# Kernel tuning notes

Hardware: AMD Instinct MI355X
Metric: run time of the kernel (lower is better)

Reference implementation:

```python
import jax, jax.numpy as jnp
import numpy as np


def setup_inputs() -> dict:
    B, S, D = 4, 4096, 256
    key = jax.random.key(0)
    ks = jax.random.split(key, 7)
    s = 1.0 / np.sqrt(D)
    return {
        "x": jax.random.normal(ks[0], (B, S, D), dtype=jnp.float32),
        "Wq": jax.random.normal(ks[1], (D, D), dtype=jnp.float32) * s,
        "bq": jnp.zeros((D,), dtype=jnp.float32),
        "Wk": jax.random.normal(ks[2], (D, D), dtype=jnp.float32) * s,
        "bk": jnp.zeros((D,), dtype=jnp.float32),
        "Wv": jax.random.normal(ks[3], (D, D), dtype=jnp.float32) * s,
        "bv": jnp.zeros((D,), dtype=jnp.float32),
    }


def reference(x, Wq, bq, Wk, bk, Wv, bv):
    # Dense projections (single head, no scaling in original)
    Q = x @ Wq + bq  # [B,S,D]
    K = x @ Wk + bk
    V = x @ Wv + bv
    scores = jnp.einsum("bsd,btd->bst", Q, K)  # [B,S,S]
    # Original takes top_k with k = seq_len, so threshold == row minimum;
    # mask 'scores >= threshold' keeps everything (no-op), kept for fidelity.
    threshold = jnp.min(scores, axis=-1, keepdims=True)
    NEG = jnp.float32(-1e9)
    sparse_scores = jnp.where(scores >= threshold, scores, NEG)
    weights = jax.nn.softmax(sparse_scores, axis=-1)
    return jnp.einsum("bst,btd->bsd", weights, V)  # [B,S,D]
```

## Files before the change

### kernel.cpp

```cpp
#include <hip/hip_runtime.h>
#include <hip/hip_fp16.h>


typedef _Float16 f16x8 __attribute__((ext_vector_type(8)));
typedef _Float16 f16x4 __attribute__((ext_vector_type(4)));
typedef __fp16   fp16x2 __attribute__((ext_vector_type(2)));
typedef float    f32x4 __attribute__((ext_vector_type(4)));
typedef float    f32x16 __attribute__((ext_vector_type(16)));

#define MFMA16(A, B, C) __builtin_amdgcn_mfma_f32_16x16x32_f16((A), (B), (C), 0, 0, 0)
#define MFMA32(A, B, C) __builtin_amdgcn_mfma_f32_32x32x16_f16((A), (B), (C), 0, 0, 0)

static __device__ __forceinline__ void gload16(const _Float16* g, _Float16* l) {
    __builtin_amdgcn_global_load_lds(
        (unsigned int __attribute__((address_space(1)))*)g,
        (unsigned int __attribute__((address_space(3)))*)l, 16, 0, 0);
}

static __device__ __forceinline__ unsigned packh(float a, float b) {
    union { fp16x2 h; unsigned u; } x;
    x.h = __builtin_amdgcn_cvt_pkrtz(a, b);
    return x.u;
}

static __device__ __forceinline__ float fexp2(float x) {
    float r;
    asm("v_exp_f32 %0, %1" : "=v"(r) : "v"(x));
    return r;
}

static __device__ __forceinline__ void load_xfrag(const float* xp, f16x8& Ah, f16x8& Al) {
    float4 a0 = *(const float4*)xp;
    float4 a1 = *(const float4*)(xp + 4);
    float v[8] = {a0.x, a0.y, a0.z, a0.w, a1.x, a1.y, a1.z, a1.w};
#pragma unroll
    for (int j = 0; j < 8; ++j) {
        _Float16 h = (_Float16)v[j];
        Ah[j] = h;
        Al[j] = (_Float16)(v[j] - (float)h);
    }
}

static __device__ __forceinline__ void load_xfrag_hi(const float* xp, f16x8& Ah) {
    float4 a0 = *(const float4*)xp;
    float4 a1 = *(const float4*)(xp + 4);
    float v[8] = {a0.x, a0.y, a0.z, a0.w, a1.x, a1.y, a1.z, a1.w};
#pragma unroll
    for (int j = 0; j < 8; ++j) Ah[j] = (_Float16)v[j];
}

__global__ __launch_bounds__(256) void convert_w_kernel(
    const float* __restrict__ Wq, const float* __restrict__ Wk, const float* __restrict__ Wv,
    _Float16* __restrict__ Wth, _Float16* __restrict__ Wtl, int* __restrict__ cnt)
{
    if (blockIdx.x == 0 && threadIdx.x < 8) cnt[threadIdx.x * 64] = 0;
    int idx = blockIdx.x * 256 + threadIdx.x;
    int mat = idx >> 16, e = idx & 65535;
    int k = e >> 8, n = e & 255;
    const float* W = (mat == 0) ? Wq : (mat == 1) ? Wk : Wv;
    float v = W[e];
    _Float16 h = (_Float16)v;
    _Float16 lo = (_Float16)(v - (float)h);
    const int lane = (n & 15) + 16 * ((k >> 3) & 3);
    const int dst = mat * 65536 + (((k >> 5) * 16 + (n >> 4)) * 64 + lane) * 8 + (k & 7);
    Wth[dst] = h;
    Wtl[dst] = lo;
}

template <int MODE>
static __device__ __forceinline__ void proj_body(
    const float* __restrict__ x, const _Float16* __restrict__ Wh,
    const _Float16* __restrict__ Wl, const float* __restrict__ bias,
    _Float16* __restrict__ dst)
{
    const int tid = threadIdx.x, wid = tid >> 6, lane = tid & 63;
    const int lrow = lane & 15, lgrp = lane >> 4;
    const int rb = blockIdx.x * 4 + wid;
    const int row0 = rb * 16;

    f32x4 acc[16];
#pragma unroll
    for (int i = 0; i < 16; ++i) acc[i] = f32x4{0.f, 0.f, 0.f, 0.f};

#pragma unroll
    for (int ks = 0; ks < 8; ++ks) {
        f16x8 Ah, Al;
        if constexpr (MODE == 2) {
            load_xfrag_hi(x + (size_t)(row0 + lrow) * 256 + ks * 32 + lgrp * 8, Ah);
        } else {
            load_xfrag(x + (size_t)(row0 + lrow) * 256 + ks * 32 + lgrp * 8, Ah, Al);
        }
#pragma unroll
        for (int nt = 0; nt < 16; ++nt) {
            const size_t bbase = ((ks * 16 + nt) * 64 + lane) * 8;
            f16x8 Bh = *(const f16x8*)(Wh + bbase);
            acc[nt] = MFMA16(Ah, Bh, acc[nt]);
            if constexpr (MODE != 2) {
                f16x8 Bl = *(const f16x8*)(Wl + bbase);
                acc[nt] = MFMA16(Al, Bh, acc[nt]);
                acc[nt] = MFMA16(Ah, Bl, acc[nt]);
            }
        }
    }

    const float LOG2E = 1.4426950408889634f;
#pragma unroll
    for (int nt = 0; nt < 16; ++nt) {
        const int n = nt * 16 + lrow;
        const float bb = bias[n];
        if constexpr (MODE == 2) {
            const int m0 = row0 + lgrp * 4;
            f16x4 vv;
#pragma unroll
            for (int r = 0; r < 4; ++r) vv[r] = (_Float16)(acc[nt][r] + bb);
            *(f16x4*)(dst + (size_t)n * 16384 + m0) = vv;
        } else {
            const float s = (MODE == 0) ? LOG2E : 1.0f;
#pragma unroll
            for (int r = 0; r < 4; ++r) {
                const int grow = row0 + lgrp * 4 + r;
                dst[(size_t)grow * 256 + n] = (_Float16)((acc[nt][r] + bb) * s);
            }
        }
    }
}

__global__ __launch_bounds__(256) void proj_all_kernel(
    const float* __restrict__ x,
    const _Float16* __restrict__ Wth, const _Float16* __restrict__ Wtl,
    const float* __restrict__ bq, const float* __restrict__ bk,
    const float* __restrict__ bv,
    _Float16* __restrict__ Qf, _Float16* __restrict__ Kf, _Float16* __restrict__ Vt)
{
    const int m = blockIdx.y;
    if (m == 0)      proj_body<0>(x, Wth,          Wtl,          bq, Qf);
    else if (m == 1) proj_body<1>(x, Wth + 65536,  Wtl + 65536,  bk, Kf);
    else             proj_body<2>(x, Wth + 131072, nullptr,      bv, Vt);
}

__global__ __launch_bounds__(256, 2) void attn8_kernel(
    const _Float16* __restrict__ Qf, const _Float16* __restrict__ Kf,
    const _Float16* __restrict__ Vt, _Float16* __restrict__ Op01,
    _Float16* __restrict__ Op23, float* __restrict__ ml, int* __restrict__ cnt)
{
    __shared__ _Float16 Kb[2][32 * 256];
    __shared__ _Float16 Vb[2][256 * 32];
    __shared__ int s_item;

    const int tid = threadIdx.x, wid = tid >> 6, lane = tid & 63;
    const int lq = lane & 31, hi = lane >> 5;

    if (tid == 0) {
        int xcd;
        asm volatile("s_getreg_b32 %0, hwreg(HW_REG_XCC_ID)" : "=s"(xcd));
        xcd &= 7;
        int item = -1;
#pragma unroll 1
        for (int k = 0; k < 8; ++k) {
            const int qidx = (xcd + k) & 7;
            int v = atomicAdd(cnt + qidx * 64, 1);
            if (v < 64) { item = qidx * 64 + v; break; }
        }
        s_item = item;
    }
    __syncthreads();
    const int item = s_item;
    const int group = (item >> 6) * 2 + ((item & 63) >> 5);
    const int qi = item & 31;
    const int b = group >> 2, split = group & 3;
    const size_t bS = (size_t)b * 4096;
    const size_t qrow = bS + qi * 128 + wid * 32;
    const size_t k0g = bS + (size_t)split * 1024;
    const int NT = 32;

    f16x8 QB[16];
#pragma unroll
    for (int ks = 0; ks < 16; ++ks)
        QB[ks] = *(const f16x8*)(Qf + (qrow + lq) * 256 + ks * 16 + hi * 8);

    f32x16 Oacc[8];
#pragma unroll
    for (int i = 0; i < 8; ++i)
#pragma unroll
        for (int r = 0; r < 16; ++r) Oacc[i][r] = 0.f;
    float m_r = -1e30f, l_r = 0.f;

    auto stage = [&](int buf, int t) {
        const size_t krow = k0g + (size_t)t * 32;
#pragma unroll
        for (int it = 0; it < 4; ++it) {
            const int s = it * 256 + tid;
            const int row = s >> 5, c = s & 31;
            const int src = c ^ (row & 7) ^ (((row >> 3) & 3) << 3);
            gload16(Kf + (krow + row) * 256 + src * 8, &Kb[buf][s * 8]);
        }
#pragma unroll
        for (int it = 0; it < 4; ++it) {
            const int s = it * 256 + tid;
            const int d = s >> 2, c = s & 3;
            gload16(Vt + (size_t)d * 16384 + krow + ((c ^ ((d >> 1) & 3)) * 8), &Vb[buf][s * 8]);
        }
    };

    stage(0, 0);
    asm volatile("s_waitcnt vmcnt(0)" ::: "memory");
    __builtin_amdgcn_s_barrier();

    const float THR = 10.0f;
    const int kx = (lq & 7) ^ (((lq >> 3) & 3) << 3);
    const int vx = (lq >> 1) & 3;
    int buf = 0;
    for (int t = 0; t < NT; ++t) {
        if (t + 1 < NT) stage(buf ^ 1, t + 1);
        const _Float16* K_ = Kb[buf];
        const _Float16* V_ = Vb[buf];

        f32x16 sc;
#pragma unroll
        for (int r = 0; r < 16; ++r) sc[r] = 0.f;
#pragma unroll
        for (int ks = 0; ks < 16; ++ks) {
            const int slot = (2 * ks + hi) ^ kx;
            f16x8 Ak = *(const f16x8*)((const char*)K_ + lq * 512 + slot * 16);
            sc = MFMA32(Ak, QB[ks], sc);
        }

        float tm[8];
#pragma unroll
        for (int j = 0; j < 8; ++j) tm[j] = fmaxf(sc[j], sc[j + 8]);
#pragma unroll
        for (int s = 4; s > 0; s >>= 1)
#pragma unroll
            for (int j = 0; j < s; ++j) tm[j] = fmaxf(tm[j], tm[j + s]);
        float mx = fmaxf(tm[0], __shfl_xor(tm[0], 32));
        if (__any(mx > m_r + THR)) {
            const float mn = fmaxf(m_r, mx);
            const float scl = fexp2(m_r - mn);
            m_r = mn; l_r *= scl;
#pragma unroll
            for (int i = 0; i < 8; ++i)
#pragma unroll
                for (int r = 0; r < 16; ++r) Oacc[i][r] *= scl;
        }

        float p[16];
#pragma unroll
        for (int r = 0; r < 16; ++r) p[r] = fexp2(sc[r] - m_r);
        float ts[8];
#pragma unroll
        for (int j = 0; j < 8; ++j) ts[j] = p[j] + p[j + 8];
#pragma unroll
        for (int s = 4; s > 0; s >>= 1)
#pragma unroll
            for (int j = 0; j < s; ++j) ts[j] += ts[j + s];
        l_r += ts[0] + __shfl_xor(ts[0], 32);

        unsigned w[8], pw[8];
#pragma unroll
        for (int j = 0; j < 8; ++j) {
            w[j] = packh(p[2 * j], p[2 * j + 1]);
            pw[j] = __shfl_xor(w[j], 32);
        }
        f16x8 Pfrag[2];
#pragma unroll
        for (int s = 0; s < 2; ++s) {
            unsigned f0 = hi ? pw[4 * s + 2] : w[4 * s + 0];
            unsigned f1 = hi ? pw[4 * s + 3] : w[4 * s + 1];
            unsigned f2 = hi ? w[4 * s + 2] : pw[4 * s + 0];
            unsigned f3 = hi ? w[4 * s + 3] : pw[4 * s + 1];
            union { unsigned u[4]; f16x8 f; } cvt;
            cvt.u[0] = f0; cvt.u[1] = f1; cvt.u[2] = f2; cvt.u[3] = f3;
            Pfrag[s] = cvt.f;
        }

#pragma unroll
        for (int dblk = 0; dblk < 8; ++dblk) {
#pragma unroll
            for (int kstep = 0; kstep < 2; ++kstep) {
                const int slot = (kstep * 2 + hi) ^ vx;
                f16x8 Av = *(const f16x8*)((const char*)V_ + (dblk * 32 + lq) * 64 + slot * 16);
                Oacc[dblk] = MFMA32(Av, Pfrag[kstep], Oacc[dblk]);
            }
        }

        asm volatile("s_waitcnt vmcnt(0)" ::: "memory");
        __builtin_amdgcn_s_barrier();
        buf ^= 1;
    }

    _Float16* Ops = (split < 2) ? (Op01 + (size_t)split * 4194304)
                                : (Op23 + (size_t)(split - 2) * 4194304);
    const float inv = 1.0f / l_r;
    const size_t grow = qrow + lq;
#pragma unroll
    for (int dblk = 0; dblk < 8; ++dblk)
#pragma unroll
        for (int quad = 0; quad < 4; ++quad) {
            f16x4 o;
#pragma unroll
            for (int j = 0; j < 4; ++j) o[j] = (_Float16)(Oacc[dblk][quad * 4 + j] * inv);
            *(f16x4*)(Ops + grow * 256 + dblk * 32 + 8 * quad + 4 * hi) = o;
        }
    if (hi == 0) {
        ml[((size_t)split * 16384 + grow) * 2]     = m_r;
        ml[((size_t)split * 16384 + grow) * 2 + 1] = l_r;
    }
}

__global__ __launch_bounds__(256) void combine_kernel(
    const _Float16* __restrict__ Op01, const _Float16* __restrict__ Op23,
    const float* __restrict__ ml, float* __restrict__ out)
{
    const int idx = blockIdx.x * 256 + threadIdx.x;
    const int row = idx >> 3, d8 = (idx & 7) * 32;
    float m_s[4], l_s[4], w[4];
    float M = -1e30f;
#pragma unroll
    for (int s = 0; s < 4; ++s) {
        m_s[s] = ml[((size_t)s * 16384 + row) * 2];
        l_s[s] = ml[((size_t)s * 16384 + row) * 2 + 1];
        M = fmaxf(M, m_s[s]);
    }
    float Wsum = 0.f;
#pragma unroll
    for (int s = 0; s < 4; ++s) { w[s] = l_s[s] * fexp2(m_s[s] - M); Wsum += w[s]; }
    const float inv = 1.0f / Wsum;
#pragma unroll
    for (int s = 0; s < 4; ++s) w[s] *= inv;

#pragma unroll
    for (int ch = 0; ch < 4; ++ch) {
        const int d0 = d8 + ch * 8;
        float acc[8] = {0.f, 0.f, 0.f, 0.f, 0.f, 0.f, 0.f, 0.f};
#pragma unroll
        for (int s = 0; s < 4; ++s) {
            const _Float16* Op = (s < 2) ? (Op01 + (size_t)s * 4194304)
                                         : (Op23 + (size_t)(s - 2) * 4194304);
            f16x8 v = *(const f16x8*)(Op + (size_t)row * 256 + d0);
#pragma unroll
            for (int j = 0; j < 8; ++j) acc[j] += w[s] * (float)v[j];
        }
        float4 o0 = {acc[0], acc[1], acc[2], acc[3]};
        float4 o1 = {acc[4], acc[5], acc[6], acc[7]};
        *(float4*)(out + (size_t)row * 256 + d0) = o0;
        *(float4*)(out + (size_t)row * 256 + d0 + 4) = o1;
    }
}

extern "C" void kernel_launch(void* const* d_in, const int* in_sizes, int n_in,
                              void* d_out, int out_size, void* d_ws, size_t ws_size,
                              hipStream_t stream) {
    const float* x  = (const float*)d_in[0];
    const float* Wq = (const float*)d_in[1];
    const float* bq = (const float*)d_in[2];
    const float* Wk = (const float*)d_in[3];
    const float* bk = (const float*)d_in[4];
    const float* Wv = (const float*)d_in[5];
    const float* bv = (const float*)d_in[6];
    float* out = (float*)d_out;

    _Float16* Op01 = (_Float16*)d_ws;
    _Float16* Qf  = Op01 + 2 * 4194304;
    _Float16* Kf  = Qf  + 4194304;
    _Float16* Vt  = Kf  + 4194304;
    _Float16* Wth = Vt  + 4194304;
    _Float16* Wtl = Wth + 196608;
    float*    ml  = (float*)(Wtl + 196608);
    _Float16* Op23 = (_Float16*)((char*)ml + 524288);
    int*      cnt = (int*)(Op23 + 2 * 4194304);

    convert_w_kernel<<<768, 256, 0, stream>>>(Wq, Wk, Wv, Wth, Wtl, cnt);
    proj_all_kernel<<<dim3(256, 3), 256, 0, stream>>>(x, Wth, Wtl, bq, bk, bv, Qf, Kf, Vt);
    attn8_kernel<<<512, 256, 0, stream>>>(Qf, Kf, Vt, Op01, Op23, ml, cnt);
    combine_kernel<<<512, 256, 0, stream>>>(Op01, Op23, ml, out);
}
```

Measured before the change: 166.9 us.

## Fuse combine into attention, drop split-fp16 projections, stage projection stores via LDS

Removes the fp16 hi/lo error-compensation terms for the Q and K projections, cutting projection MFMAs threefold and dropping the low-part weight buffer. The weight conversion kernel now writes whole 8-element fragments per thread. Projection outputs are staged through LDS so global stores are coalesced 16-byte writes. The separate combine kernel is replaced by a last-block-done pattern inside the attention kernel using a done counter and threadfence. This saves a launch but loses some precision on Q and K.

New measurement: 242.6 us. +45.3%, slower.

```diff
diff --git a/kernel.cpp b/kernel.cpp
--- a/kernel.cpp
+++ b/kernel.cpp
@@ -29,18 +29,6 @@
     return r;
 }
 
-static __device__ __forceinline__ void load_xfrag(const float* xp, f16x8& Ah, f16x8& Al) {
-    float4 a0 = *(const float4*)xp;
-    float4 a1 = *(const float4*)(xp + 4);
-    float v[8] = {a0.x, a0.y, a0.z, a0.w, a1.x, a1.y, a1.z, a1.w};
-#pragma unroll
-    for (int j = 0; j < 8; ++j) {
-        _Float16 h = (_Float16)v[j];
-        Ah[j] = h;
-        Al[j] = (_Float16)(v[j] - (float)h);
-    }
-}
-
 static __device__ __forceinline__ void load_xfrag_hi(const float* xp, f16x8& Ah) {
     float4 a0 = *(const float4*)xp;
     float4 a1 = *(const float4*)(xp + 4);
@@ -51,27 +39,30 @@
 
 __global__ __launch_bounds__(256) void convert_w_kernel(
     const float* __restrict__ Wq, const float* __restrict__ Wk, const float* __restrict__ Wv,
-    _Float16* __restrict__ Wth, _Float16* __restrict__ Wtl, int* __restrict__ cnt)
+    _Float16* __restrict__ Wth, int* __restrict__ cnt, int* __restrict__ done)
 {
-    if (blockIdx.x == 0 && threadIdx.x < 8) cnt[threadIdx.x * 64] = 0;
+    if (blockIdx.x == 0) {
+        if (threadIdx.x < 8)   cnt[threadIdx.x * 64] = 0;
+        if (threadIdx.x < 128) done[threadIdx.x * 16] = 0;
+    }
     int idx = blockIdx.x * 256 + threadIdx.x;
-    int mat = idx >> 16, e = idx & 65535;
-    int k = e >> 8, n = e & 255;
+    int mat = idx >> 13, f_l = idx & 8191;
+    int frag = f_l >> 6, lane = f_l & 63;
+    int ks = frag >> 4, nt = frag & 15;
+    int n = nt * 16 + (lane & 15);
+    int k0 = ks * 32 + ((lane >> 4) & 3) * 8;
     const float* W = (mat == 0) ? Wq : (mat == 1) ? Wk : Wv;
-    float v = W[e];
-    _Float16 h = (_Float16)v;
-    _Float16 lo = (_Float16)(v - (float)h);
-    const int lane = (n & 15) + 16 * ((k >> 3) & 3);
-    const int dst = mat * 65536 + (((k >> 5) * 16 + (n >> 4)) * 64 + lane) * 8 + (k & 7);
-    Wth[dst] = h;
-    Wtl[dst] = lo;
+    f16x8 h;
+#pragma unroll
+    for (int j = 0; j < 8; ++j) h[j] = (_Float16)W[(k0 + j) * 256 + n];
+    *(f16x8*)(Wth + mat * 65536 + (size_t)f_l * 8) = h;
 }
 
 template <int MODE>
 static __device__ __forceinline__ void proj_body(
     const float* __restrict__ x, const _Float16* __restrict__ Wh,
-    const _Float16* __restrict__ Wl, const float* __restrict__ bias,
-    _Float16* __restrict__ dst)
+    const float* __restrict__ bias, _Float16* __restrict__ dst,
+    _Float16* __restrict__ lds)
 {
     const int tid = threadIdx.x, wid = tid >> 6, lane = tid & 63;
     const int lrow = lane & 15, lgrp = lane >> 4;
@@ -84,64 +75,77 @@
 
 #pragma unroll
     for (int ks = 0; ks < 8; ++ks) {
-        f16x8 Ah, Al;
-        if constexpr (MODE == 2) {
-            load_xfrag_hi(x + (size_t)(row0 + lrow) * 256 + ks * 32 + lgrp * 8, Ah);
-        } else {
-            load_xfrag(x + (size_t)(row0 + lrow) * 256 + ks * 32 + lgrp * 8, Ah, Al);
-        }
+        f16x8 Ah;
+        load_xfrag_hi(x + (size_t)(row0 + lrow) * 256 + ks * 32 + lgrp * 8, Ah);
 #pragma unroll
         for (int nt = 0; nt < 16; ++nt) {
-            const size_t bbase = ((ks * 16 + nt) * 64 + lane) * 8;
-            f16x8 Bh = *(const f16x8*)(Wh + bbase);
+            f16x8 Bh = *(const f16x8*)(Wh + ((ks * 16 + nt) * 64 + lane) * 8);
             acc[nt] = MFMA16(Ah, Bh, acc[nt]);
-            if constexpr (MODE != 2) {
-                f16x8 Bl = *(const f16x8*)(Wl + bbase);
-                acc[nt] = MFMA16(Al, Bh, acc[nt]);
-                acc[nt] = MFMA16(Ah, Bl, acc[nt]);
+        }
+    }
+
+    const float LOG2E = 1.4426950408889634f;
+    if constexpr (MODE == 2) {
+        const int m_l = wid * 16 + lgrp * 4;
+        const int cm = m_l >> 3, oic = (lgrp & 1) * 4;
+#pragma unroll
+        for (int nt = 0; nt < 16; ++nt) {
+            const int n = nt * 16 + lrow;
+            const float bb = bias[n];
+            f16x4 v;
+#pragma unroll
+            for (int r = 0; r < 4; ++r) v[r] = (_Float16)(acc[nt][r] + bb);
+            *(f16x4*)(lds + n * 72 + (cm ^ (n & 7)) * 8 + oic) = v;
+        }
+        __syncthreads();
+#pragma unroll
+        for (int it = 0; it < 8; ++it) {
+            const int u = it * 256 + tid;
+            const int n = u >> 3, c = u & 7;
+            f16x8 v = *(const f16x8*)(lds + n * 72 + ((c ^ (n & 7))) * 8);
+            *(f16x8*)(dst + (size_t)n * 16384 + blockIdx.x * 64 + c * 8) = v;
+        }
+    } else {
+        const float s = (MODE == 0) ? LOG2E : 1.0f;
+#pragma unroll
+        for (int nt = 0; nt < 16; ++nt) {
+            const int n = nt * 16 + lrow;
+            const float bb = bias[n];
+#pragma unroll
+            for (int r = 0; r < 4; ++r) {
+                const int row_l = wid * 16 + lgrp * 4 + r;
+                lds[row_l * 264 + n] = (_Float16)((acc[nt][r] + bb) * s);
             }
         }
-    }
-
-    const float LOG2E = 1.4426950408889634f;
-#pragma unroll
-    for (int nt = 0; nt < 16; ++nt) {
-        const int n = nt * 16 + lrow;
-        const float bb = bias[n];
-        if constexpr (MODE == 2) {
-            const int m0 = row0 + lgrp * 4;
-            f16x4 vv;
-#pragma unroll
-            for (int r = 0; r < 4; ++r) vv[r] = (_Float16)(acc[nt][r] + bb);
-            *(f16x4*)(dst + (size_t)n * 16384 + m0) = vv;
-        } else {
-            const float s = (MODE == 0) ? LOG2E : 1.0f;
-#pragma unroll
-            for (int r = 0; r < 4; ++r) {
-                const int grow = row0 + lgrp * 4 + r;
-                dst[(size_t)grow * 256 + n] = (_Float16)((acc[nt][r] + bb) * s);
-            }
+        __syncthreads();
+#pragma unroll
+        for (int it = 0; it < 8; ++it) {
+            const int u = it * 256 + tid;
+            const int row_l = u >> 5, c = u & 31;
+            f16x8 v = *(const f16x8*)(lds + row_l * 264 + c * 8);
+            *(f16x8*)(dst + ((size_t)blockIdx.x * 64 + row_l) * 256 + c * 8) = v;
         }
     }
 }
 
 __global__ __launch_bounds__(256) void proj_all_kernel(
-    const float* __restrict__ x,
-    const _Float16* __restrict__ Wth, const _Float16* __restrict__ Wtl,
+    const float* __restrict__ x, const _Float16* __restrict__ Wth,
     const float* __restrict__ bq, const float* __restrict__ bk,
     const float* __restrict__ bv,
     _Float16* __restrict__ Qf, _Float16* __restrict__ Kf, _Float16* __restrict__ Vt)
 {
+    __shared__ _Float16 lds[18432];
     const int m = blockIdx.y;
-    if (m == 0)      proj_body<0>(x, Wth,          Wtl,          bq, Qf);
-    else if (m == 1) proj_body<1>(x, Wth + 65536,  Wtl + 65536,  bk, Kf);
-    else             proj_body<2>(x, Wth + 131072, nullptr,      bv, Vt);
+    if (m == 0)      proj_body<0>(x, Wth,          bq, Qf, lds);
+    else if (m == 1) proj_body<1>(x, Wth + 65536,  bk, Kf, lds);
+    else             proj_body<2>(x, Wth + 131072, bv, Vt, lds);
 }
 
 __global__ __launch_bounds__(256, 2) void attn8_kernel(
     const _Float16* __restrict__ Qf, const _Float16* __restrict__ Kf,
     const _Float16* __restrict__ Vt, _Float16* __restrict__ Op01,
-    _Float16* __restrict__ Op23, float* __restrict__ ml, int* __restrict__ cnt)
+    _Float16* __restrict__ Op23, float* __restrict__ ml, int* __restrict__ cnt,
+    int* __restrict__ done, float* __restrict__ out)
 {
     __shared__ _Float16 Kb[2][32 * 256];
     __shared__ _Float16 Vb[2][256 * 32];
@@ -305,45 +309,48 @@
         ml[((size_t)split * 16384 + grow) * 2]     = m_r;
         ml[((size_t)split * 16384 + grow) * 2 + 1] = l_r;
     }
-}
-
-__global__ __launch_bounds__(256) void combine_kernel(
-    const _Float16* __restrict__ Op01, const _Float16* __restrict__ Op23,
-    const float* __restrict__ ml, float* __restrict__ out)
-{
-    const int idx = blockIdx.x * 256 + threadIdx.x;
-    const int row = idx >> 3, d8 = (idx & 7) * 32;
-    float m_s[4], l_s[4], w[4];
-    float M = -1e30f;
-#pragma unroll
-    for (int s = 0; s < 4; ++s) {
-        m_s[s] = ml[((size_t)s * 16384 + row) * 2];
-        l_s[s] = ml[((size_t)s * 16384 + row) * 2 + 1];
-        M = fmaxf(M, m_s[s]);
-    }
-    float Wsum = 0.f;
-#pragma unroll
-    for (int s = 0; s < 4; ++s) { w[s] = l_s[s] * fexp2(m_s[s] - M); Wsum += w[s]; }
-    const float inv = 1.0f / Wsum;
-#pragma unroll
-    for (int s = 0; s < 4; ++s) w[s] *= inv;
-
-#pragma unroll
-    for (int ch = 0; ch < 4; ++ch) {
-        const int d0 = d8 + ch * 8;
-        float acc[8] = {0.f, 0.f, 0.f, 0.f, 0.f, 0.f, 0.f, 0.f};
-#pragma unroll
-        for (int s = 0; s < 4; ++s) {
-            const _Float16* Op = (s < 2) ? (Op01 + (size_t)s * 4194304)
-                                         : (Op23 + (size_t)(s - 2) * 4194304);
-            f16x8 v = *(const f16x8*)(Op + (size_t)row * 256 + d0);
-#pragma unroll
-            for (int j = 0; j < 8; ++j) acc[j] += w[s] * (float)v[j];
-        }
-        float4 o0 = {acc[0], acc[1], acc[2], acc[3]};
-        float4 o1 = {acc[4], acc[5], acc[6], acc[7]};
-        *(float4*)(out + (size_t)row * 256 + d0) = o0;
-        *(float4*)(out + (size_t)row * 256 + d0 + 4) = o1;
+
+    __threadfence();
+    __shared__ int s_last;
+    if (tid == 0) {
+        const int gid = b * 32 + qi;
+        s_last = (atomicAdd(done + gid * 16, 1) == 3);
+    }
+    __syncthreads();
+    if (s_last) {
+        __threadfence();
+        const size_t row0g = bS + (size_t)qi * 128;
+        const int rbase = tid >> 5;
+        const int c0 = (tid & 31) * 8;
+#pragma unroll 1
+        for (int rr = 0; rr < 16; ++rr) {
+            const size_t row = row0g + rbase * 16 + rr;
+            float m_s[4], l_s[4], wgt[4];
+            float M = -1e30f;
+#pragma unroll
+            for (int s = 0; s < 4; ++s) {
+                m_s[s] = ml[((size_t)s * 16384 + row) * 2];
+                l_s[s] = ml[((size_t)s * 16384 + row) * 2 + 1];
+                M = fmaxf(M, m_s[s]);
+            }
+            float Wsum = 0.f;
+#pragma unroll
+            for (int s = 0; s < 4; ++s) { wgt[s] = l_s[s] * fexp2(m_s[s] - M); Wsum += wgt[s]; }
+            const float winv = 1.0f / Wsum;
+            float acc2[8] = {0.f, 0.f, 0.f, 0.f, 0.f, 0.f, 0.f, 0.f};
+#pragma unroll
+            for (int s = 0; s < 4; ++s) {
+                const _Float16* Op = (s < 2) ? (Op01 + (size_t)s * 4194304)
+                                             : (Op23 + (size_t)(s - 2) * 4194304);
+                f16x8 v = *(const f16x8*)(Op + row * 256 + c0);
+#pragma unroll
+                for (int j = 0; j < 8; ++j) acc2[j] += wgt[s] * (float)v[j];
+            }
+            float4 o0 = {acc2[0] * winv, acc2[1] * winv, acc2[2] * winv, acc2[3] * winv};
+            float4 o1 = {acc2[4] * winv, acc2[5] * winv, acc2[6] * winv, acc2[7] * winv};
+            *(float4*)(out + row * 256 + c0) = o0;
+            *(float4*)(out + row * 256 + c0 + 4) = o1;
+        }
     }
 }
 
@@ -364,13 +371,12 @@
     _Float16* Kf  = Qf  + 4194304;
     _Float16* Vt  = Kf  + 4194304;
     _Float16* Wth = Vt  + 4194304;
-    _Float16* Wtl = Wth + 196608;
-    float*    ml  = (float*)(Wtl + 196608);
+    float*    ml  = (float*)(Wth + 196608);
     _Float16* Op23 = (_Float16*)((char*)ml + 524288);
-    int*      cnt = (int*)(Op23 + 2 * 4194304);
-
-    convert_w_kernel<<<768, 256, 0, stream>>>(Wq, Wk, Wv, Wth, Wtl, cnt);
-    proj_all_kernel<<<dim3(256, 3), 256, 0, stream>>>(x, Wth, Wtl, bq, bk, bv, Qf, Kf, Vt);
-    attn8_kernel<<<512, 256, 0, stream>>>(Qf, Kf, Vt, Op01, Op23, ml, cnt);
-    combine_kernel<<<512, 256, 0, stream>>>(Op01, Op23, ml, out);
-}
+    int*      cnt  = (int*)(Op23 + 2 * 4194304);
+    int*      done = cnt + 512;
+
+    convert_w_kernel<<<96, 256, 0, stream>>>(Wq, Wk, Wv, Wth, cnt, done);
+    proj_all_kernel<<<dim3(256, 3), 256, 0, stream>>>(x, Wth, bq, bk, bv, Qf, Kf, Vt);
+    attn8_kernel<<<512, 256, 0, stream>>>(Qf, Kf, Vt, Op01, Op23, ml, cnt, done, out);
+}
```
